# Kernel tuning notes

Hardware: AMD Instinct MI355X
Metric: run time of the kernel (lower is better)

Reference implementation:

```python
import jax, jax.numpy as jnp
import numpy as np

WIDTH, HEIGHT = 256, 256
FOV = 1.0471975511965976  # 60 deg horizontal fov, radians
Z_NEAR, Z_FAR = 2.0, 6.0
NUM_SAMPLES = 64
HIDDEN = 64


def get_cam_ray_dirs(width, height, horizontal_fov):
    rot_y = jnp.linspace(-horizontal_fov / 2.0, horizontal_fov / 2.0, width)
    vfov = horizontal_fov * height / width
    rot_x = jnp.linspace(vfov / 2.0, -vfov / 2.0, height)
    rot_y = jnp.broadcast_to(rot_y[None, :], (height, width))
    rot_x = jnp.broadcast_to(rot_x[:, None], (height, width))
    x = -jnp.sin(rot_y) * jnp.cos(rot_x)
    y = jnp.sin(rot_x)
    z = -jnp.cos(rot_y) * jnp.cos(rot_x)
    return jnp.stack([x, y, z], axis=2)  # (H, W, 3)


def setup_inputs() -> dict:
    key = jax.random.key(0)
    k1, k2, k3, k4, k5 = jax.random.split(key, 5)
    camera_local_to_world = jax.random.normal(k1, (4, 4), dtype=jnp.float32)
    u = jax.random.uniform(k2, (HEIGHT * WIDTH, NUM_SAMPLES), dtype=jnp.float32)
    cam_ray_dirs = get_cam_ray_dirs(WIDTH, HEIGHT, FOV).astype(jnp.float32)
    W1 = jax.random.normal(k3, (6, HIDDEN), dtype=jnp.float32) * 0.4
    b1 = jnp.zeros((HIDDEN,), dtype=jnp.float32)
    W2 = jax.random.normal(k4, (HIDDEN, 4), dtype=jnp.float32) * 0.1
    b2 = jnp.zeros((4,), dtype=jnp.float32)
    return {"camera_local_to_world": camera_local_to_world, "u": u,
            "cam_ray_dirs": cam_ray_dirs, "W1": W1, "b1": b1, "W2": W2, "b2": b2}


def reference(camera_local_to_world, u, cam_ray_dirs, W1, b1, W2, b2):
    H, W, _ = cam_ray_dirs.shape
    R = H * W
    S = u.shape[1]

    # world-space rays
    rot = camera_local_to_world[:3, :3]
    ray_origin = camera_local_to_world[:3, 3]                    # (3,)
    ray_dirs = jnp.einsum('ij,hwj->hwi', rot, cam_ray_dirs).reshape(R, 3)

    # binned-uniform sample distances along each ray
    dt = Z_FAR - Z_NEAR
    bin_dt = dt / S
    t = jnp.linspace(Z_NEAR, Z_FAR - bin_dt, S, dtype=jnp.float32)[None, :] + u * bin_dt  # (R, S)

    # sample positions and view directions
    pos = ray_origin[None, None, :] + ray_dirs[:, None, :] * t[:, :, None]   # (R, S, 3)
    dirs = jnp.broadcast_to(ray_dirs[:, None, :], (R, S, 3))
    x = jnp.concatenate([pos.reshape(R * S, 3), dirs.reshape(R * S, 3)], axis=1)  # (R*S, 6)

    # radiance MLP: density (non-negative) + rgb color
    h = jax.nn.relu(x @ W1 + b1)                 # (R*S, HIDDEN)
    out = h @ W2 + b2                            # (R*S, 4)
    densities = jax.nn.relu(out[:, 0]).reshape(R, S)
    colors = jax.nn.sigmoid(out[:, 1:]).reshape(R, S, 3)

    # alpha compositing (vectorized form of the back-to-front recurrence:
    # weight_i = alpha_i * prod_{j<i}(1 - alpha_j))
    seps = t[:, 1:] - t[:, :-1]                                   # (R, S-1)
    alphas = 1.0 - jnp.exp(-densities[:, :-1] * seps)             # (R, S-1)
    last_alpha = 1.0 - jnp.exp(-densities[:, -1:] * bin_dt)       # mean_sample_separation = bin_dt
    a = jnp.concatenate([alphas, last_alpha], axis=1)             # (R, S)
    trans = jnp.cumprod(1.0 - a, axis=1)
    T = jnp.concatenate([jnp.ones((R, 1), a.dtype), trans[:, :-1]], axis=1)  # exclusive cumprod
    weights = a * T                                               # (R, S)
    color = jnp.sum(weights[:, :, None] * colors, axis=1)         # (R, 3)
    return color.reshape(H, W, 3)
```

## Files before the change

kernel.cpp:

```cpp
#include <hip/hip_runtime.h>

#define NUM_SAMPLES 64
#define HIDDEN 64
#define Z_NEAR 2.0f
#define Z_FAR 6.0f
#define RPW 8

typedef _Float16 half8 __attribute__((ext_vector_type(8)));
typedef __fp16  fp16x2 __attribute__((ext_vector_type(2)));
typedef float   float4t __attribute__((ext_vector_type(4)));

template<int CTRL, int RMASK>
__device__ __forceinline__ float dpp_add(float x) {
    const int m = __builtin_amdgcn_update_dpp(0, __float_as_int(x), CTRL, RMASK, 0xf, true);
    return x + __int_as_float(m);
}
__device__ __forceinline__ float wave_scan_add(float x) {
    x = dpp_add<0x111, 0xf>(x);
    x = dpp_add<0x112, 0xf>(x);
    x = dpp_add<0x114, 0xf>(x);
    x = dpp_add<0x118, 0xf>(x);
    x = dpp_add<0x142, 0xa>(x);
    x = dpp_add<0x143, 0xc>(x);
    return x;
}

#define LOG2E 1.44269504088896f

__global__ __launch_bounds__(256, 8) void render_kernel(
    const float* __restrict__ cam,
    const float* __restrict__ u,
    const float* __restrict__ cdirs,
    const float* __restrict__ W1,
    const float* __restrict__ b1,
    const float* __restrict__ W2,
    const float* __restrict__ b2,
    float* __restrict__ out)
{
    const int lane = threadIdx.x & 63;
    const int wid  = threadIdx.x >> 6;
    const int wave = blockIdx.x * 4 + wid;
    const int grp  = lane >> 4;
    const int col  = lane & 15;

    __shared__ __align__(16) __fp16 Ahsh[4][HIDDEN];
    __shared__ __align__(16) __fp16 Bhsh[4][HIDDEN];
    __shared__ __align__(16) float  tsh[4][NUM_SAMPLES];
    __shared__ __align__(16) __fp16 W2T[4][4][80];
    __shared__ float cst[4][NUM_SAMPLES * 5];

    {
        const float4 w2row = ((const float4*)W2)[lane];
        W2T[wid][0][lane] = (__fp16)w2row.x;
        W2T[wid][1][lane] = (__fp16)w2row.y;
        W2T[wid][2][lane] = (__fp16)w2row.z;
        W2T[wid][3][lane] = (__fp16)w2row.w;
    }

    const float cl = (lane < 12) ? cam[lane] : 0.0f;
    float camv[12];
    #pragma unroll
    for (int i = 0; i < 12; ++i)
        camv[i] = __int_as_float(__builtin_amdgcn_readlane(__float_as_int(cl), i));

    const float w10 = W1[0*HIDDEN+lane], w11 = W1[1*HIDDEN+lane], w12 = W1[2*HIDDEN+lane];
    const float w13 = W1[3*HIDDEN+lane], w14 = W1[4*HIDDEN+lane], w15 = W1[5*HIDDEN+lane];
    const float b1h = b1[lane];
    const float b2v = b2[col & 3];

    half8 bfrag[2] = {};
    if (col < 4) {
        bfrag[0] = *(const half8*)(&W2T[wid][col][grp*8]);
        bfrag[1] = *(const half8*)(&W2T[wid][col][32 + grp*8]);
    }

    const float bin_dt = (Z_FAR - Z_NEAR) / (float)NUM_SAMPLES;
    const fp16x2 hzero = {(__fp16)0.0f, (__fp16)0.0f};

    int ray = wave * RPW;
    float uv  = u[ray*NUM_SAMPLES + lane];
    float cd0 = cdirs[ray*3+0], cd1 = cdirs[ray*3+1], cd2 = cdirs[ray*3+2];

    for (int it = 0; it < RPW; ++it, ++ray) {
        float uv_n = 0.f, cd0_n = 0.f, cd1_n = 0.f, cd2_n = 0.f;
        if (it < RPW-1) {
            uv_n  = u[(ray+1)*NUM_SAMPLES + lane];
            cd0_n = cdirs[(ray+1)*3+0];
            cd1_n = cdirs[(ray+1)*3+1];
            cd2_n = cdirs[(ray+1)*3+2];
        }

        const float rd0 = fmaf(camv[0], cd0, fmaf(camv[1], cd1, camv[2]*cd2));
        const float rd1 = fmaf(camv[4], cd0, fmaf(camv[5], cd1, camv[6]*cd2));
        const float rd2 = fmaf(camv[8], cd0, fmaf(camv[9], cd1, camv[10]*cd2));
        const float o0 = camv[3], o1 = camv[7], o2 = camv[11];

        {
            const float A = fmaf(rd0, w10, fmaf(rd1, w11, rd2*w12));
            float B = fmaf(o0, w10, fmaf(o1, w11, o2*w12));
            B = fmaf(rd0, w13, fmaf(rd1, w14, fmaf(rd2, w15, B))) + b1h;
            Ahsh[wid][lane] = (__fp16)A;
            Bhsh[wid][lane] = (__fp16)B;
        }

        const float t = fmaf((float)lane + uv, bin_dt, Z_NEAR);
        tsh[wid][lane] = t;

        union { fp16x2 h2[4]; half8 h8; } aAh[2], aBh[2];
        #pragma unroll
        for (int kt = 0; kt < 2; ++kt) {
            const int h0 = kt*32 + grp*8;
            aAh[kt].h8 = *(const half8*)(&Ahsh[wid][h0]);
            aBh[kt].h8 = *(const half8*)(&Bhsh[wid][h0]);
        }

        const float tn  = tsh[wid][(lane+1) & 63];
        const float sep = (lane < NUM_SAMPLES-1) ? (tn - t) : bin_dt;

        #pragma unroll
        for (int m = 0; m < 4; ++m) {
            const float tm = tsh[wid][col + 16*m];
            const fp16x2 tvh = __builtin_amdgcn_cvt_pkrtz(tm, tm);
            float4t c = {b2v, b2v, b2v, b2v};
            #pragma unroll
            for (int kt = 0; kt < 2; ++kt) {
                union { fp16x2 h2[4]; half8 h8; } au;
                #pragma unroll
                for (int q = 0; q < 4; ++q) {
                    const fp16x2 pre = __builtin_elementwise_fma(aAh[kt].h2[q], tvh, aBh[kt].h2[q]);
                    au.h2[q] = __builtin_elementwise_max(pre, hzero);
                }
                c = __builtin_amdgcn_mfma_f32_16x16x32_f16(au.h8, bfrag[kt], c, 0, 0, 0);
            }
            if (col < 4) {
                #pragma unroll
                for (int r = 0; r < 4; ++r) {
                    const int sample = 16*m + grp*4 + r;
                    cst[wid][sample*5 + col] = c[r];
                }
            }
        }

        const float acc0 = cst[wid][lane*5 + 0];
        const float acc1 = cst[wid][lane*5 + 1];
        const float acc2 = cst[wid][lane*5 + 2];
        const float acc3 = cst[wid][lane*5 + 3];

        const float density = fmaxf(acc0, 0.0f);
        const float dsep  = density * sep;
        const float lg    = -dsep * LOG2E;
        const float alpha = 1.0f - __builtin_amdgcn_exp2f(lg);
        const float S     = wave_scan_add(lg);
        const float T     = __builtin_amdgcn_exp2f(S - lg);
        const float w     = alpha * T;

        float c0 = w * __builtin_amdgcn_rcpf(1.0f + __builtin_amdgcn_exp2f(-acc1 * LOG2E));
        float c1 = w * __builtin_amdgcn_rcpf(1.0f + __builtin_amdgcn_exp2f(-acc2 * LOG2E));
        float c2 = w * __builtin_amdgcn_rcpf(1.0f + __builtin_amdgcn_exp2f(-acc3 * LOG2E));
        c0 = wave_scan_add(c0);
        c1 = wave_scan_add(c1);
        c2 = wave_scan_add(c2);
        if (lane == 63) {
            out[ray*3+0] = c0;
            out[ray*3+1] = c1;
            out[ray*3+2] = c2;
        }

        uv = uv_n; cd0 = cd0_n; cd1 = cd1_n; cd2 = cd2_n;
    }
}

extern "C" void kernel_launch(void* const* d_in, const int* in_sizes, int n_in,
                              void* d_out, int out_size, void* d_ws, size_t ws_size,
                              hipStream_t stream) {
    const float* cam   = (const float*)d_in[0];
    const float* u     = (const float*)d_in[1];
    const float* cdirs = (const float*)d_in[2];
    const float* W1    = (const float*)d_in[3];
    const float* b1    = (const float*)d_in[4];
    const float* W2    = (const float*)d_in[5];
    const float* b2    = (const float*)d_in[6];
    float* out = (float*)d_out;

    dim3 grid(2048), block(256);
    render_kernel<<<grid, block, 0, stream>>>(cam, u, cdirs, W1, b1, W2, b2, out);
}
```

Baseline: 33.37 us.

## Map one ray per wave, swap MFMA operands, and load W2 directly

Each wave now processes a single ray instead of looping over eight, so the grid grows to one block per four rays. The W2 fragment is built straight from global memory with packed conversions, removing the per-wave shared transpose. The MFMA operands are swapped so the four outputs land in one lane's accumulator as a float4 and are written with a vector store. The b2 bias is added after the matmul, and t values are computed in registers rather than read back from shared memory. This trades the per-wave prefetch pipelining and reuse of the setup work across rays for more parallelism and fewer shared-memory scatter stores, at the cost of repeating the setup (W1, W2 and camera loads) for every ray.

```diff
diff --git a/kernel.cpp b/kernel.cpp
--- a/kernel.cpp
+++ b/kernel.cpp
@@ -4,7 +4,7 @@
 #define HIDDEN 64
 #define Z_NEAR 2.0f
 #define Z_FAR 6.0f
-#define RPW 8
+#define LOG2E 1.44269504088896f
 
 typedef _Float16 half8 __attribute__((ext_vector_type(8)));
 typedef __fp16  fp16x2 __attribute__((ext_vector_type(2)));
@@ -25,9 +25,9 @@
     return x;
 }
 
-#define LOG2E 1.44269504088896f
+__device__ __forceinline__ int slot16(int s) { return 2*s + ((s>>2)&1); }
 
-__global__ __launch_bounds__(256, 8) void render_kernel(
+__global__ __launch_bounds__(256) void render_kernel(
     const float* __restrict__ cam,
     const float* __restrict__ u,
     const float* __restrict__ cdirs,
@@ -39,23 +39,14 @@
 {
     const int lane = threadIdx.x & 63;
     const int wid  = threadIdx.x >> 6;
-    const int wave = blockIdx.x * 4 + wid;
+    const int ray  = blockIdx.x * 4 + wid;
     const int grp  = lane >> 4;
     const int col  = lane & 15;
 
     __shared__ __align__(16) __fp16 Ahsh[4][HIDDEN];
     __shared__ __align__(16) __fp16 Bhsh[4][HIDDEN];
     __shared__ __align__(16) float  tsh[4][NUM_SAMPLES];
-    __shared__ __align__(16) __fp16 W2T[4][4][80];
-    __shared__ float cst[4][NUM_SAMPLES * 5];
-
-    {
-        const float4 w2row = ((const float4*)W2)[lane];
-        W2T[wid][0][lane] = (__fp16)w2row.x;
-        W2T[wid][1][lane] = (__fp16)w2row.y;
-        W2T[wid][2][lane] = (__fp16)w2row.z;
-        W2T[wid][3][lane] = (__fp16)w2row.w;
-    }
+    __shared__ __align__(16) float  cst[4][NUM_SAMPLES * 8];
 
     const float cl = (lane < 12) ? cam[lane] : 0.0f;
     float camv[12];
@@ -66,107 +57,100 @@
     const float w10 = W1[0*HIDDEN+lane], w11 = W1[1*HIDDEN+lane], w12 = W1[2*HIDDEN+lane];
     const float w13 = W1[3*HIDDEN+lane], w14 = W1[4*HIDDEN+lane], w15 = W1[5*HIDDEN+lane];
     const float b1h = b1[lane];
-    const float b2v = b2[col & 3];
+    const float b20 = b2[0], b21 = b2[1], b22 = b2[2], b23 = b2[3];
 
-    half8 bfrag[2] = {};
+    half8 wfrag[2] = {};
     if (col < 4) {
-        bfrag[0] = *(const half8*)(&W2T[wid][col][grp*8]);
-        bfrag[1] = *(const half8*)(&W2T[wid][col][32 + grp*8]);
+        const float* wp = W2 + (grp*8)*4 + col;
+        union { fp16x2 h2[4]; half8 h8; } w0, w1;
+        #pragma unroll
+        for (int q = 0; q < 4; ++q) {
+            w0.h2[q] = __builtin_amdgcn_cvt_pkrtz(wp[(q*2  )*4], wp[(q*2+1)*4]);
+            w1.h2[q] = __builtin_amdgcn_cvt_pkrtz(wp[(32+q*2)*4], wp[(32+q*2+1)*4]);
+        }
+        wfrag[0] = w0.h8;
+        wfrag[1] = w1.h8;
+    }
+
+    const float* up = u + ray*NUM_SAMPLES + col;
+    const float u0 = up[0], u1 = up[16], u2 = up[32], u3 = up[48];
+    const float uown = (grp & 2) ? ((grp & 1) ? u3 : u2) : ((grp & 1) ? u1 : u0);
+
+    const float cd0 = cdirs[ray*3+0], cd1 = cdirs[ray*3+1], cd2 = cdirs[ray*3+2];
+    const float rd0 = fmaf(camv[0], cd0, fmaf(camv[1], cd1, camv[2]*cd2));
+    const float rd1 = fmaf(camv[4], cd0, fmaf(camv[5], cd1, camv[6]*cd2));
+    const float rd2 = fmaf(camv[8], cd0, fmaf(camv[9], cd1, camv[10]*cd2));
+    const float o0 = camv[3], o1 = camv[7], o2 = camv[11];
+
+    {
+        const float A = fmaf(rd0, w10, fmaf(rd1, w11, rd2*w12));
+        float B = fmaf(o0, w10, fmaf(o1, w11, o2*w12));
+        B = fmaf(rd0, w13, fmaf(rd1, w14, fmaf(rd2, w15, B))) + b1h;
+        Ahsh[wid][lane] = (__fp16)A;
+        Bhsh[wid][lane] = (__fp16)B;
     }
 
     const float bin_dt = (Z_FAR - Z_NEAR) / (float)NUM_SAMPLES;
+    const float t = fmaf((float)lane + uown, bin_dt, Z_NEAR);
+    tsh[wid][lane] = t;
+
+    union { fp16x2 h2[4]; half8 h8; } aAh[2], aBh[2];
+    #pragma unroll
+    for (int kt = 0; kt < 2; ++kt) {
+        const int h0 = kt*32 + grp*8;
+        aAh[kt].h8 = *(const half8*)(&Ahsh[wid][h0]);
+        aBh[kt].h8 = *(const half8*)(&Bhsh[wid][h0]);
+    }
+
+    const float tn  = tsh[wid][(lane+1) & 63];
+    const float sep = (lane < NUM_SAMPLES-1) ? (tn - t) : bin_dt;
+
     const fp16x2 hzero = {(__fp16)0.0f, (__fp16)0.0f};
 
-    int ray = wave * RPW;
-    float uv  = u[ray*NUM_SAMPLES + lane];
-    float cd0 = cdirs[ray*3+0], cd1 = cdirs[ray*3+1], cd2 = cdirs[ray*3+2];
-
-    for (int it = 0; it < RPW; ++it, ++ray) {
-        float uv_n = 0.f, cd0_n = 0.f, cd1_n = 0.f, cd2_n = 0.f;
-        if (it < RPW-1) {
-            uv_n  = u[(ray+1)*NUM_SAMPLES + lane];
-            cd0_n = cdirs[(ray+1)*3+0];
-            cd1_n = cdirs[(ray+1)*3+1];
-            cd2_n = cdirs[(ray+1)*3+2];
-        }
-
-        const float rd0 = fmaf(camv[0], cd0, fmaf(camv[1], cd1, camv[2]*cd2));
-        const float rd1 = fmaf(camv[4], cd0, fmaf(camv[5], cd1, camv[6]*cd2));
-        const float rd2 = fmaf(camv[8], cd0, fmaf(camv[9], cd1, camv[10]*cd2));
-        const float o0 = camv[3], o1 = camv[7], o2 = camv[11];
-
-        {
-            const float A = fmaf(rd0, w10, fmaf(rd1, w11, rd2*w12));
-            float B = fmaf(o0, w10, fmaf(o1, w11, o2*w12));
-            B = fmaf(rd0, w13, fmaf(rd1, w14, fmaf(rd2, w15, B))) + b1h;
-            Ahsh[wid][lane] = (__fp16)A;
-            Bhsh[wid][lane] = (__fp16)B;
-        }
-
-        const float t = fmaf((float)lane + uv, bin_dt, Z_NEAR);
-        tsh[wid][lane] = t;
-
-        union { fp16x2 h2[4]; half8 h8; } aAh[2], aBh[2];
+    #pragma unroll
+    for (int m = 0; m < 4; ++m) {
+        const float um = (m == 0) ? u0 : (m == 1) ? u1 : (m == 2) ? u2 : u3;
+        const float tm = fmaf((float)(16*m + col) + um, bin_dt, Z_NEAR);
+        const fp16x2 tvh = __builtin_amdgcn_cvt_pkrtz(tm, tm);
+        float4t c = {0.f, 0.f, 0.f, 0.f};
         #pragma unroll
         for (int kt = 0; kt < 2; ++kt) {
-            const int h0 = kt*32 + grp*8;
-            aAh[kt].h8 = *(const half8*)(&Ahsh[wid][h0]);
-            aBh[kt].h8 = *(const half8*)(&Bhsh[wid][h0]);
+            union { fp16x2 h2[4]; half8 h8; } au;
+            #pragma unroll
+            for (int q = 0; q < 4; ++q) {
+                const fp16x2 pre = __builtin_elementwise_fma(aAh[kt].h2[q], tvh, aBh[kt].h2[q]);
+                au.h2[q] = __builtin_elementwise_max(pre, hzero);
+            }
+            c = __builtin_amdgcn_mfma_f32_16x16x32_f16(wfrag[kt], au.h8, c, 0, 0, 0);
         }
+        if (lane < 16)
+            *(float4t*)(&cst[wid][slot16(16*m + lane) * 4]) = c;
+    }
 
-        const float tn  = tsh[wid][(lane+1) & 63];
-        const float sep = (lane < NUM_SAMPLES-1) ? (tn - t) : bin_dt;
+    const float4t c4 = *(const float4t*)(&cst[wid][slot16(lane) * 4]);
+    const float acc0 = c4[0] + b20;
+    const float acc1 = c4[1] + b21;
+    const float acc2 = c4[2] + b22;
+    const float acc3 = c4[3] + b23;
 
-        #pragma unroll
-        for (int m = 0; m < 4; ++m) {
-            const float tm = tsh[wid][col + 16*m];
-            const fp16x2 tvh = __builtin_amdgcn_cvt_pkrtz(tm, tm);
-            float4t c = {b2v, b2v, b2v, b2v};
-            #pragma unroll
-            for (int kt = 0; kt < 2; ++kt) {
-                union { fp16x2 h2[4]; half8 h8; } au;
-                #pragma unroll
-                for (int q = 0; q < 4; ++q) {
-                    const fp16x2 pre = __builtin_elementwise_fma(aAh[kt].h2[q], tvh, aBh[kt].h2[q]);
-                    au.h2[q] = __builtin_elementwise_max(pre, hzero);
-                }
-                c = __builtin_amdgcn_mfma_f32_16x16x32_f16(au.h8, bfrag[kt], c, 0, 0, 0);
-            }
-            if (col < 4) {
-                #pragma unroll
-                for (int r = 0; r < 4; ++r) {
-                    const int sample = 16*m + grp*4 + r;
-                    cst[wid][sample*5 + col] = c[r];
-                }
-            }
-        }
+    const float density = fmaxf(acc0, 0.0f);
+    const float dsep  = density * sep;
+    const float lg    = -dsep * LOG2E;
+    const float alpha = 1.0f - __builtin_amdgcn_exp2f(lg);
+    const float S     = wave_scan_add(lg);
+    const float T     = __builtin_amdgcn_exp2f(S - lg);
+    const float w     = alpha * T;
 
-        const float acc0 = cst[wid][lane*5 + 0];
-        const float acc1 = cst[wid][lane*5 + 1];
-        const float acc2 = cst[wid][lane*5 + 2];
-        const float acc3 = cst[wid][lane*5 + 3];
-
-        const float density = fmaxf(acc0, 0.0f);
-        const float dsep  = density * sep;
-        const float lg    = -dsep * LOG2E;
-        const float alpha = 1.0f - __builtin_amdgcn_exp2f(lg);
-        const float S     = wave_scan_add(lg);
-        const float T     = __builtin_amdgcn_exp2f(S - lg);
-        const float w     = alpha * T;
-
-        float c0 = w * __builtin_amdgcn_rcpf(1.0f + __builtin_amdgcn_exp2f(-acc1 * LOG2E));
-        float c1 = w * __builtin_amdgcn_rcpf(1.0f + __builtin_amdgcn_exp2f(-acc2 * LOG2E));
-        float c2 = w * __builtin_amdgcn_rcpf(1.0f + __builtin_amdgcn_exp2f(-acc3 * LOG2E));
-        c0 = wave_scan_add(c0);
-        c1 = wave_scan_add(c1);
-        c2 = wave_scan_add(c2);
-        if (lane == 63) {
-            out[ray*3+0] = c0;
-            out[ray*3+1] = c1;
-            out[ray*3+2] = c2;
-        }
-
-        uv = uv_n; cd0 = cd0_n; cd1 = cd1_n; cd2 = cd2_n;
+    float c0 = w * __builtin_amdgcn_rcpf(1.0f + __builtin_amdgcn_exp2f(-acc1 * LOG2E));
+    float c1 = w * __builtin_amdgcn_rcpf(1.0f + __builtin_amdgcn_exp2f(-acc2 * LOG2E));
+    float c2 = w * __builtin_amdgcn_rcpf(1.0f + __builtin_amdgcn_exp2f(-acc3 * LOG2E));
+    c0 = wave_scan_add(c0);
+    c1 = wave_scan_add(c1);
+    c2 = wave_scan_add(c2);
+    if (lane == 63) {
+        out[ray*3+0] = c0;
+        out[ray*3+1] = c1;
+        out[ray*3+2] = c2;
     }
 }
 
@@ -182,6 +166,7 @@
     const float* b2    = (const float*)d_in[6];
     float* out = (float*)d_out;
 
-    dim3 grid(2048), block(256);
+    const int R = 256 * 256;
+    dim3 grid(R / 4), block(256);
     render_kernel<<<grid, block, 0, stream>>>(cam, u, cdirs, W1, b1, W2, b2, out);
 }
```

Result: no change. 33.85 us (+1.4%).
